# Kernel tuning notes

Hardware: AMD Instinct MI355X
Metric: run time of the kernel (lower is better)

The kernel has to match this reference:

```python
import jax, jax.numpy as jnp
import numpy as np

N, E, D, H = 50000, 800000, 64, 4  # nodes, edges, dim_h, heads
NEG_SLOPE = 0.2
BN_EPS = 1e-5


def setup_inputs() -> dict:
    key = jax.random.key(0)
    ks = jax.random.split(key, 8)
    x = jax.random.normal(ks[0], (N, D), dtype=jnp.float32)
    edge_index = jax.random.randint(ks[1], (2, E), 0, N, dtype=jnp.int32)
    s = 1.0 / np.sqrt(D)
    W_lin = jax.random.normal(ks[2], (D, D), dtype=jnp.float32) * s
    b_lin = jnp.zeros((D,), dtype=jnp.float32)
    prelu_w = jnp.full((D,), 0.25, dtype=jnp.float32)
    W_gat = jax.random.normal(ks[3], (H * D, D), dtype=jnp.float32) * s  # maps D -> H*D
    att_src = jax.random.normal(ks[4], (H, D), dtype=jnp.float32) * 0.1
    att_dst = jax.random.normal(ks[5], (H, D), dtype=jnp.float32) * 0.1
    gat_bias = jnp.zeros((D,), dtype=jnp.float32)
    bn_gamma = jnp.ones((D,), dtype=jnp.float32)
    bn_beta = jnp.zeros((D,), dtype=jnp.float32)
    return dict(x=x, edge_index=edge_index, W_lin=W_lin, b_lin=b_lin,
                prelu_w=prelu_w, W_gat=W_gat, att_src=att_src, att_dst=att_dst,
                gat_bias=gat_bias, bn_gamma=bn_gamma, bn_beta=bn_beta)


def _gat_mod_fwd(x, edge_index, W_lin, b_lin, prelu_w, W_gat, att_src, att_dst,
                 gat_bias, bn_gamma, bn_beta):
    # --- pre linear + PReLU ---
    x = x @ W_lin.T + b_lin
    x = jnp.where(x >= 0, x, prelu_w * x)  # per-channel PReLU

    # --- GATConv (concat=False -> head mean), add_self_loops=True ---
    h = (x @ W_gat.T).reshape(N, H, D)              # [N,H,D]
    a_src = jnp.einsum('nhd,hd->nh', h, att_src)    # [N,H]
    a_dst = jnp.einsum('nhd,hd->nh', h, att_dst)    # [N,H]

    loop = jnp.arange(N, dtype=edge_index.dtype)
    src = jnp.concatenate([edge_index[0], loop])    # [E+N]
    dst = jnp.concatenate([edge_index[1], loop])

    e = jax.nn.leaky_relu(a_src[src] + a_dst[dst], NEG_SLOPE)   # [E+N, H]
    # segment softmax over destination nodes (self loops guarantee non-empty)
    emax = jax.ops.segment_max(e, dst, num_segments=N)          # [N,H]
    p = jnp.exp(e - emax[dst])
    denom = jax.ops.segment_sum(p, dst, num_segments=N)         # [N,H]
    alpha = p / denom[dst]                                      # [E+N,H]

    msg = h[src] * alpha[:, :, None]                            # [E+N,H,D]
    out = jax.ops.segment_sum(msg, dst, num_segments=N)         # [N,H,D]
    out = out.mean(axis=1) + gat_bias                           # [N,D]

    # --- BatchNorm1d (training: batch stats) + ReLU ---
    mean = out.mean(axis=0)
    var = out.var(axis=0)
    out = bn_gamma * (out - mean) * jax.lax.rsqrt(var + BN_EPS) + bn_beta
    return jax.nn.relu(out)


def reference(x, edge_index, W_lin, b_lin, prelu_w, W_gat, att_src, att_dst,
              gat_bias, bn_gamma, bn_beta):
    return _gat_mod_fwd(x, edge_index, W_lin, b_lin, prelu_w, W_gat, att_src,
                        att_dst, gat_bias, bn_gamma, bn_beta)
```

## Files before the change

### kernel.cpp

```cpp
#include <hip/hip_runtime.h>
#include <hip/hip_fp16.h>

#define NEG_SLOPE 0.2f
#define BN_EPS 1e-5f

constexpr int D = 64;
constexpr int H = 4;

typedef _Float16 half2_t __attribute__((ext_vector_type(2)));
typedef _Float16 half4_t __attribute__((ext_vector_type(4)));
typedef _Float16 half8_t __attribute__((ext_vector_type(8)));
typedef float f32x4_t __attribute__((ext_vector_type(4)));
typedef int i32x4 __attribute__((ext_vector_type(4)));

union Rec {
    i32x4 i4;
    struct { int idx; int pad; half4_t w; } f;
};

#define MFMA16(a, b, c) __builtin_amdgcn_mfma_f32_16x16x32_f16(a, b, c, 0, 0, 0)

#if __has_builtin(__builtin_amdgcn_fdot2)
#define FDOT2(a, b, c) __builtin_amdgcn_fdot2((a), (b), (c), false)
#else
#define FDOT2(a, b, c) ((c) + (float)(a)[0] * (float)(b)[0] + (float)(a)[1] * (float)(b)[1])
#endif

__device__ inline half2_t h2cast(unsigned int u) { return __builtin_bit_cast(half2_t, u); }

__device__ inline float lrelu(float v) { return (v >= 0.f) ? v : NEG_SLOPE * v; }

__device__ inline void split8(const float* p, bool ok, half8_t& hi, half8_t& lo) {
    float f[8];
    if (ok) {
        float4 a = *(const float4*)p;
        float4 b = *(const float4*)(p + 4);
        f[0] = a.x; f[1] = a.y; f[2] = a.z; f[3] = a.w;
        f[4] = b.x; f[5] = b.y; f[6] = b.z; f[7] = b.w;
    } else {
        #pragma unroll
        for (int j = 0; j < 8; j++) f[j] = 0.f;
    }
    #pragma unroll
    for (int j = 0; j < 8; j++) {
        _Float16 h = (_Float16)f[j];
        hi[j] = h;
        lo[j] = (_Float16)(f[j] - (float)h);
    }
}

__global__ __launch_bounds__(256) void k_node(
    const float* __restrict__ x,
    const float* __restrict__ W_lin, const float* __restrict__ b_lin,
    const float* __restrict__ prelu_w, const float* __restrict__ W_gat,
    const float* __restrict__ att_src, const float* __restrict__ att_dst,
    _Float16* __restrict__ hh, float* __restrict__ asrc_ws,
    float* __restrict__ adst_ws, const int* __restrict__ ei,
    int* __restrict__ deg8, int* __restrict__ rank, int N, int E)
{
    __shared__ _Float16 smem[32 * 264];
    _Float16* __restrict__ h_lds = smem;
    _Float16* __restrict__ x1hi  = smem;
    _Float16* __restrict__ x1lo  = smem + 32 * 72;

    const int t = threadIdx.x;
    const int w = t >> 6;
    const int l = t & 63;
    const int li = l & 15;
    const int lq = l >> 4;
    const int base = blockIdx.x * 32;
    const int nvalid = min(32, N - base);

    const int nthreads = gridDim.x * 256;
    const int e0 = blockIdx.x * 256 + t;
    const int e1 = e0 + nthreads;
    const bool v0 = e0 < E;
    const bool v1 = e1 < E;
    const int xcd = blockIdx.x & 7;
    int r0v = 0, r1v = 0;
    {
        int d0 = 0, d1 = 0;
        if (v0) d0 = ei[E + e0];
        if (v1) d1 = ei[E + e1];
        if (v0) r0v = atomicAdd(&deg8[xcd * N + d0], 1);
        if (v1) r1v = atomicAdd(&deg8[xcd * N + d1], 1);
    }

    f32x4_t accA[2] = {};
    {
        half8_t blh[2], bll[2];
        const int n = 16 * w + li;
        #pragma unroll
        for (int ks = 0; ks < 2; ks++)
            split8(W_lin + n * 64 + 32 * ks + 8 * lq, true, blh[ks], bll[ks]);
        #pragma unroll
        for (int mt = 0; mt < 2; mt++) {
            const int row = base + 16 * mt + li;
            const bool ok = row < N;
            #pragma unroll
            for (int ks = 0; ks < 2; ks++) {
                half8_t ah, al;
                split8(x + (size_t)row * 64 + 32 * ks + 8 * lq, ok, ah, al);
                accA[mt] = MFMA16(ah, blh[ks], accA[mt]);
                accA[mt] = MFMA16(al, blh[ks], accA[mt]);
                accA[mt] = MFMA16(ah, bll[ks], accA[mt]);
            }
        }
    }

    if (v0) rank[e0] = r0v;
    if (v1) rank[e1] = r1v;

    {
        const int n = 16 * w + li;
        const float bl = b_lin[n];
        const float pw = prelu_w[n];
        #pragma unroll
        for (int mt = 0; mt < 2; mt++) {
            #pragma unroll
            for (int r = 0; r < 4; r++) {
                const int m = 16 * mt + lq * 4 + r;
                float v = accA[mt][r] + bl;
                v = (v >= 0.f) ? v : pw * v;
                _Float16 hi = (_Float16)v;
                x1hi[m * 72 + n] = hi;
                x1lo[m * 72 + n] = (_Float16)(v - (float)hi);
            }
        }
    }
    __syncthreads();

    half8_t xah[2][2], xal[2][2];
    #pragma unroll
    for (int mt = 0; mt < 2; mt++) {
        #pragma unroll
        for (int ks = 0; ks < 2; ks++) {
            const int off = (16 * mt + li) * 72 + 32 * ks + 8 * lq;
            xah[mt][ks] = *(const half8_t*)(&x1hi[off]);
            xal[mt][ks] = *(const half8_t*)(&x1lo[off]);
        }
    }
    f32x4_t accB[2][4] = {};
    #pragma unroll
    for (int nt = 0; nt < 4; nt++) {
        half8_t wh[2], wl[2];
        const int c = 64 * w + 16 * nt + li;
        #pragma unroll
        for (int ks = 0; ks < 2; ks++)
            split8(W_gat + (size_t)c * 64 + 32 * ks + 8 * lq, true, wh[ks], wl[ks]);
        #pragma unroll
        for (int mt = 0; mt < 2; mt++) {
            #pragma unroll
            for (int ks = 0; ks < 2; ks++) {
                accB[mt][nt] = MFMA16(xah[mt][ks], wh[ks], accB[mt][nt]);
                accB[mt][nt] = MFMA16(xal[mt][ks], wh[ks], accB[mt][nt]);
                accB[mt][nt] = MFMA16(xah[mt][ks], wl[ks], accB[mt][nt]);
            }
        }
    }

    {
        float asv[4], adv[4];
        #pragma unroll
        for (int nt = 0; nt < 4; nt++) {
            const int c = 64 * w + 16 * nt + li;
            asv[nt] = att_src[c];
            adv[nt] = att_dst[c];
        }
        #pragma unroll
        for (int mt = 0; mt < 2; mt++) {
            #pragma unroll
            for (int r = 0; r < 4; r++) {
                float s = 0.f, dsum = 0.f;
                #pragma unroll
                for (int nt = 0; nt < 4; nt++) {
                    s += accB[mt][nt][r] * asv[nt];
                    dsum += accB[mt][nt][r] * adv[nt];
                }
                #pragma unroll
                for (int off = 1; off < 16; off <<= 1) {
                    s += __shfl_xor(s, off, 64);
                    dsum += __shfl_xor(dsum, off, 64);
                }
                if (li == 0) {
                    const int m = 16 * mt + lq * 4 + r;
                    if (m < nvalid) {
                        asrc_ws[(size_t)(base + m) * H + w] = s;
                        adst_ws[(size_t)(base + m) * H + w] = dsum;
                    }
                }
            }
        }
    }

    __syncthreads();

    #pragma unroll
    for (int mt = 0; mt < 2; mt++) {
        #pragma unroll
        for (int nt = 0; nt < 4; nt++) {
            #pragma unroll
            for (int r = 0; r < 4; r++) {
                const int m = 16 * mt + lq * 4 + r;
                const int d = 16 * nt + li;
                h_lds[m * 264 + d * 4 + w] = (_Float16)accB[mt][nt][r];
            }
        }
    }
    __syncthreads();
    {
        const int chunks = nvalid * 32;
        const uint4* src = (const uint4*)h_lds;
        uint4* dst = (uint4*)(hh + (size_t)base * 256);
        for (int i = t; i < chunks; i += 256) {
            int row = i >> 5;
            int col = i & 31;
            dst[i] = src[row * 33 + col];
        }
    }
}

__global__ __launch_bounds__(256) void k_offsets(const int* __restrict__ deg8,
                                                 int* __restrict__ pref8,
                                                 int* __restrict__ deg,
                                                 int* __restrict__ gcount,
                                                 int* __restrict__ offs, int N) {
    __shared__ int sm[256];
    __shared__ int sbase;
    int t = threadIdx.x;
    int idx = blockIdx.x * 256 + t;
    int v = 0;
    if (idx < N) {
        #pragma unroll
        for (int p = 0; p < 8; p++) {
            int c = deg8[p * N + idx];
            pref8[p * N + idx] = v;
            v += c;
        }
        deg[idx] = v;
    }
    sm[t] = v;
    __syncthreads();
    for (int off = 1; off < 256; off <<= 1) {
        int w = (t >= off) ? sm[t - off] : 0;
        __syncthreads();
        sm[t] += w;
        __syncthreads();
    }
    if (t == 255) sbase = atomicAdd(gcount, sm[255]);
    __syncthreads();
    if (idx < N) offs[idx] = sbase + sm[t] - v;
}

__global__ __launch_bounds__(256) void k_fill(const int* __restrict__ ei,
                                              const int* __restrict__ offs,
                                              const int* __restrict__ pref8,
                                              const int* __restrict__ rank,
                                              const float* __restrict__ asrc,
                                              const float* __restrict__ adst,
                                              i32x4* __restrict__ recs,
                                              int N, int E, int NB) {
    int e = blockIdx.x * 256 + threadIdx.x;
    if (e >= E) return;
    int s = ei[e];
    int d = ei[E + e];
    int g = e >> 8;
    int p = (g < NB ? g : g - NB) & 7;
    int r0 = rank[e];
    int pos = offs[d] + pref8[p * N + d] + r0;
    float4 a = *(const float4*)(asrc + (size_t)s * H);
    float4 b = *(const float4*)(adst + (size_t)d * H);
    Rec r;
    r.f.idx = s;
    r.f.pad = 0;
    r.f.w[0] = (_Float16)__expf(lrelu(a.x + b.x));
    r.f.w[1] = (_Float16)__expf(lrelu(a.y + b.y));
    r.f.w[2] = (_Float16)__expf(lrelu(a.z + b.z));
    r.f.w[3] = (_Float16)__expf(lrelu(a.w + b.w));
    recs[pos] = r.i4;
}

__device__ inline void edge_pair(const i32x4 ra, const i32x4 rb,
                                 const uint2 ha, const uint2 hb,
                                 float& den0, float& den1, float& den2, float& den3,
                                 float& acc0, float& acc1, float& acc2, float& acc3)
{
    const half2_t one2 = h2cast(0x3C003C00u);
    unsigned int wp0 = __builtin_amdgcn_perm((unsigned int)rb.z, (unsigned int)ra.z, 0x05040100u);
    unsigned int wp1 = __builtin_amdgcn_perm((unsigned int)rb.z, (unsigned int)ra.z, 0x07060302u);
    unsigned int wp2 = __builtin_amdgcn_perm((unsigned int)rb.w, (unsigned int)ra.w, 0x05040100u);
    unsigned int wp3 = __builtin_amdgcn_perm((unsigned int)rb.w, (unsigned int)ra.w, 0x07060302u);
    unsigned int hp0 = __builtin_amdgcn_perm(hb.x, ha.x, 0x05040100u);
    unsigned int hp1 = __builtin_amdgcn_perm(hb.x, ha.x, 0x07060302u);
    unsigned int hp2 = __builtin_amdgcn_perm(hb.y, ha.y, 0x05040100u);
    unsigned int hp3 = __builtin_amdgcn_perm(hb.y, ha.y, 0x07060302u);
    den0 = FDOT2(h2cast(wp0), one2, den0);
    den1 = FDOT2(h2cast(wp1), one2, den1);
    den2 = FDOT2(h2cast(wp2), one2, den2);
    den3 = FDOT2(h2cast(wp3), one2, den3);
    acc0 = FDOT2(h2cast(wp0), h2cast(hp0), acc0);
    acc1 = FDOT2(h2cast(wp1), h2cast(hp1), acc1);
    acc2 = FDOT2(h2cast(wp2), h2cast(hp2), acc2);
    acc3 = FDOT2(h2cast(wp3), h2cast(hp3), acc3);
}

__global__ __launch_bounds__(256) void k_agg(
    const float* __restrict__ asrc, const float* __restrict__ adst,
    const int* __restrict__ offs, const int* __restrict__ deg,
    const i32x4* __restrict__ recs, const uint2* __restrict__ hh2,
    float* __restrict__ out, int N)
{
    int wid = (blockIdx.x * 256 + threadIdx.x) >> 6;
    int lane = threadIdx.x & 63;
    if (wid >= N) return;
    const int i = wid;

    float4 b = *(const float4*)(adst + (size_t)i * H);
    float4 a0 = *(const float4*)(asrc + (size_t)i * H);
    float ws0 = __expf(lrelu(a0.x + b.x));
    float ws1 = __expf(lrelu(a0.y + b.y));
    float ws2 = __expf(lrelu(a0.z + b.z));
    float ws3 = __expf(lrelu(a0.w + b.w));

    const int beg = __builtin_amdgcn_readfirstlane(offs[i]);
    const int dg  = __builtin_amdgcn_readfirstlane(deg[i]);

    float den0 = ws0, den1 = ws1, den2 = ws2, den3 = ws3;
    float acc0, acc1, acc2, acc3;
    {
        uint2 hv = hh2[(size_t)i * D + lane];
        half2_t s01 = h2cast(hv.x), s23 = h2cast(hv.y);
        acc0 = ws0 * (float)s01[0];
        acc1 = ws1 * (float)s01[1];
        acc2 = ws2 * (float)s23[0];
        acc3 = ws3 * (float)s23[1];
    }

    const int nfull = dg & ~7;
    int k = 0;
    for (; k < nfull; k += 8) {
        i32x4 rr[8];
        #pragma unroll
        for (int j = 0; j < 8; j++)
            rr[j] = __builtin_nontemporal_load(recs + beg + k + j);
        uint2 hv[8];
        #pragma unroll
        for (int j = 0; j < 8; j++)
            hv[j] = hh2[(size_t)rr[j].x * D + lane];
        #pragma unroll
        for (int j = 0; j < 8; j += 2)
            edge_pair(rr[j], rr[j + 1], hv[j], hv[j + 1],
                      den0, den1, den2, den3, acc0, acc1, acc2, acc3);
    }
    if (k < dg) {
        i32x4 rr[8];
        #pragma unroll
        for (int j = 0; j < 8; j++) {
            int kk = min(k + j, dg - 1);
            i32x4 r = __builtin_nontemporal_load(recs + beg + kk);
            if (k + j >= dg) { r.z = 0; r.w = 0; }
            rr[j] = r;
        }
        uint2 hv[8];
        #pragma unroll
        for (int j = 0; j < 8; j++)
            hv[j] = hh2[(size_t)rr[j].x * D + lane];
        #pragma unroll
        for (int j = 0; j < 8; j += 2)
            edge_pair(rr[j], rr[j + 1], hv[j], hv[j + 1],
                      den0, den1, den2, den3, acc0, acc1, acc2, acc3);
    }

    out[(size_t)i * D + lane] =
        0.25f * (acc0 / den0 + acc1 / den1 + acc2 / den2 + acc3 / den3);
}

__global__ __launch_bounds__(256) void k_bn_stats(const float* __restrict__ out,
                                                  float* __restrict__ sums,
                                                  int total) {
    const int t = threadIdx.x;
    const int stride = gridDim.x * 256;
    float s = 0.f, sq = 0.f;
    for (int idx = blockIdx.x * 256 + t; idx < total; idx += stride) {
        float v = out[idx];
        s += v;
        sq += v * v;
    }
    __shared__ float ls[256], lq[256];
    ls[t] = s;
    lq[t] = sq;
    __syncthreads();
    if (t < 64) {
        s = ls[t] + ls[t + 64] + ls[t + 128] + ls[t + 192];
        sq = lq[t] + lq[t + 64] + lq[t + 128] + lq[t + 192];
        atomicAdd(&sums[t], s);
        atomicAdd(&sums[64 + t], sq);
    }
}

__global__ __launch_bounds__(256) void k_bn_apply(float* __restrict__ out,
                                                  const float* __restrict__ sums,
                                                  const float* __restrict__ gamma,
                                                  const float* __restrict__ beta,
                                                  int total, float invN) {
    int idx = blockIdx.x * 256 + threadIdx.x;
    if (idx >= total) return;
    int c = idx & 63;
    float mean = sums[c] * invN;
    float var = sums[64 + c] * invN - mean * mean;
    float y = gamma[c] * (out[idx] - mean) * rsqrtf(var + BN_EPS) + beta[c];
    out[idx] = fmaxf(y, 0.f);
}

extern "C" void kernel_launch(void* const* d_in, const int* in_sizes, int n_in,
                              void* d_out, int out_size, void* d_ws, size_t ws_size,
                              hipStream_t stream) {
    const float* x       = (const float*)d_in[0];
    const int*   ei      = (const int*)d_in[1];
    const float* W_lin   = (const float*)d_in[2];
    const float* b_lin   = (const float*)d_in[3];
    const float* prelu_w = (const float*)d_in[4];
    const float* W_gat   = (const float*)d_in[5];
    const float* att_src = (const float*)d_in[6];
    const float* att_dst = (const float*)d_in[7];
    const float* bn_gamma = (const float*)d_in[9];
    const float* bn_beta  = (const float*)d_in[10];
    float* out = (float*)d_out;

    const int N = in_sizes[0] / D;
    const int E = in_sizes[1] / 2;

    char* wp = (char*)d_ws;
    _Float16* hh = (_Float16*)wp;      wp += (size_t)N * D * H * sizeof(_Float16);
    float* asrc  = (float*)wp;          wp += (size_t)N * H * sizeof(float);
    float* adst  = (float*)wp;          wp += (size_t)N * H * sizeof(float);
    char* zero_base = wp;
    float* sums  = (float*)wp;          wp += 2 * D * sizeof(float);
    int* deg8    = (int*)wp;            wp += (size_t)8 * N * sizeof(int);
    int* gcount  = (int*)wp;            wp += 4 * sizeof(int);
    size_t zero_bytes = (size_t)(wp - zero_base);
    int* pref8   = (int*)wp;            wp += (size_t)8 * N * sizeof(int);
    int* deg     = (int*)wp;            wp += (size_t)N * sizeof(int);
    int* offs    = (int*)wp;            wp += (size_t)N * sizeof(int);
    int* rank    = (int*)wp;            wp += (size_t)E * sizeof(int);
    i32x4* recs  = (i32x4*)wp;          wp += ((size_t)E + 4) * sizeof(i32x4);
    (void)ws_size; (void)n_in; (void)out_size;

    const int total = N * D;
    const int NB = (N + 255) / 256;
    const int NB1 = (N + 31) / 32;

    hipMemsetAsync(zero_base, 0, zero_bytes, stream);
    hipLaunchKernelGGL(k_node, dim3(NB1), dim3(256), 0, stream,
                       x, W_lin, b_lin, prelu_w, W_gat, att_src, att_dst,
                       hh, asrc, adst, ei, deg8, rank, N, E);
    hipLaunchKernelGGL(k_offsets, dim3(NB), dim3(256), 0, stream,
                       deg8, pref8, deg, gcount, offs, N);
    hipLaunchKernelGGL(k_fill, dim3((E + 255) / 256), dim3(256), 0, stream,
                       ei, offs, pref8, rank, asrc, adst, recs, N, E, NB1);
    hipLaunchKernelGGL(k_agg, dim3((N + 3) / 4), dim3(256), 0, stream,
                       asrc, adst, offs, deg, recs, (const uint2*)hh, out, N);
    hipLaunchKernelGGL(k_bn_stats, dim3(1024), dim3(256), 0, stream,
                       out, sums, total);
    hipLaunchKernelGGL(k_bn_apply, dim3((total + 255) / 256), dim3(256), 0, stream,
                       out, sums, bn_gamma, bn_beta, total, 1.f / (float)N);
}
```

Baseline: 262.7 us.

## Replace global-atomic CSR build with two-level bucketed counting sort

Drops the per-edge global atomics on per-XCD degree arrays and the rank array. The CSR is now built with a block-local LDS histogram over 32-node buckets, a three-kernel scan, a scatter into bucket order, and a per-bucket local sort into node order. It also reuses the output buffer as scratch for the intermediate records. The aim is to remove contended global atomics and scattered rank traffic. The cost is more kernel launches and an extra pass over the edge records, and the scratch reuse ties correctness to the output buffer being large enough.

```diff
diff --git a/kernel.cpp b/kernel.cpp
--- a/kernel.cpp
+++ b/kernel.cpp
@@ -6,6 +6,7 @@
 
 constexpr int D = 64;
 constexpr int H = 4;
+constexpr int MAXBUK = 1600;
 
 typedef _Float16 half2_t __attribute__((ext_vector_type(2)));
 typedef _Float16 half4_t __attribute__((ext_vector_type(4)));
@@ -55,8 +56,7 @@
     const float* __restrict__ prelu_w, const float* __restrict__ W_gat,
     const float* __restrict__ att_src, const float* __restrict__ att_dst,
     _Float16* __restrict__ hh, float* __restrict__ asrc_ws,
-    float* __restrict__ adst_ws, const int* __restrict__ ei,
-    int* __restrict__ deg8, int* __restrict__ rank, int N, int E)
+    float* __restrict__ adst_ws, int N)
 {
     __shared__ _Float16 smem[32 * 264];
     _Float16* __restrict__ h_lds = smem;
@@ -70,21 +70,6 @@
     const int lq = l >> 4;
     const int base = blockIdx.x * 32;
     const int nvalid = min(32, N - base);
-
-    const int nthreads = gridDim.x * 256;
-    const int e0 = blockIdx.x * 256 + t;
-    const int e1 = e0 + nthreads;
-    const bool v0 = e0 < E;
-    const bool v1 = e1 < E;
-    const int xcd = blockIdx.x & 7;
-    int r0v = 0, r1v = 0;
-    {
-        int d0 = 0, d1 = 0;
-        if (v0) d0 = ei[E + e0];
-        if (v1) d1 = ei[E + e1];
-        if (v0) r0v = atomicAdd(&deg8[xcd * N + d0], 1);
-        if (v1) r1v = atomicAdd(&deg8[xcd * N + d1], 1);
-    }
 
     f32x4_t accA[2] = {};
     {
@@ -107,9 +92,6 @@
             }
         }
     }
-
-    if (v0) rank[e0] = r0v;
-    if (v1) rank[e1] = r1v;
 
     {
         const int n = 16 * w + li;
@@ -220,64 +202,161 @@
     }
 }
 
-__global__ __launch_bounds__(256) void k_offsets(const int* __restrict__ deg8,
-                                                 int* __restrict__ pref8,
-                                                 int* __restrict__ deg,
-                                                 int* __restrict__ gcount,
-                                                 int* __restrict__ offs, int N) {
+__global__ __launch_bounds__(256) void k_hist(const int* __restrict__ ei,
+                                              int* __restrict__ gcnt,
+                                              int E, int chunk, int NBUK) {
+    __shared__ int cnt[MAXBUK];
+    const int p = blockIdx.x;
+    const int t = threadIdx.x;
+    for (int b = t; b < NBUK; b += 256) cnt[b] = 0;
+    __syncthreads();
+    const int e0 = p * chunk;
+    const int e1 = min(E, e0 + chunk);
+    for (int e = e0 + t; e < e1; e += 256) {
+        int d = ei[E + e];
+        atomicAdd(&cnt[d >> 5], 1);
+    }
+    __syncthreads();
+    for (int b = t; b < NBUK; b += 256) gcnt[(size_t)b * 256 + p] = cnt[b];
+}
+
+__global__ __launch_bounds__(256) void k_scan1(const int* __restrict__ gcnt,
+                                               int* __restrict__ tot, int NBUK) {
+    const int b = blockIdx.x * 4 + (threadIdx.x >> 6);
+    const int l = threadIdx.x & 63;
+    if (b >= NBUK) return;
+    int4 v = ((const int4*)(gcnt + (size_t)b * 256))[l];
+    int s = v.x + v.y + v.z + v.w;
+    #pragma unroll
+    for (int off = 1; off < 64; off <<= 1) s += __shfl_xor(s, off, 64);
+    if (l == 0) tot[b] = s;
+}
+
+__global__ __launch_bounds__(256) void k_scan2(const int* __restrict__ tot,
+                                               int* __restrict__ base, int NBUK) {
     __shared__ int sm[256];
-    __shared__ int sbase;
-    int t = threadIdx.x;
-    int idx = blockIdx.x * 256 + t;
-    int v = 0;
-    if (idx < N) {
-        #pragma unroll
-        for (int p = 0; p < 8; p++) {
-            int c = deg8[p * N + idx];
-            pref8[p * N + idx] = v;
-            v += c;
-        }
-        deg[idx] = v;
-    }
-    sm[t] = v;
-    __syncthreads();
-    for (int off = 1; off < 256; off <<= 1) {
-        int w = (t >= off) ? sm[t - off] : 0;
+    __shared__ int carry_s;
+    const int t = threadIdx.x;
+    if (t == 0) carry_s = 0;
+    __syncthreads();
+    for (int c0 = 0; c0 < NBUK; c0 += 256) {
+        const int i = c0 + t;
+        const int v = (i < NBUK) ? tot[i] : 0;
+        sm[t] = v;
         __syncthreads();
-        sm[t] += w;
+        for (int off = 1; off < 256; off <<= 1) {
+            int u = (t >= off) ? sm[t - off] : 0;
+            __syncthreads();
+            sm[t] += u;
+            __syncthreads();
+        }
+        const int inc = sm[t];
+        const int cc = carry_s;
         __syncthreads();
-    }
-    if (t == 255) sbase = atomicAdd(gcount, sm[255]);
-    __syncthreads();
-    if (idx < N) offs[idx] = sbase + sm[t] - v;
-}
-
-__global__ __launch_bounds__(256) void k_fill(const int* __restrict__ ei,
-                                              const int* __restrict__ offs,
-                                              const int* __restrict__ pref8,
-                                              const int* __restrict__ rank,
-                                              const float* __restrict__ asrc,
-                                              const float* __restrict__ adst,
-                                              i32x4* __restrict__ recs,
-                                              int N, int E, int NB) {
-    int e = blockIdx.x * 256 + threadIdx.x;
-    if (e >= E) return;
-    int s = ei[e];
-    int d = ei[E + e];
-    int g = e >> 8;
-    int p = (g < NB ? g : g - NB) & 7;
-    int r0 = rank[e];
-    int pos = offs[d] + pref8[p * N + d] + r0;
-    float4 a = *(const float4*)(asrc + (size_t)s * H);
-    float4 b = *(const float4*)(adst + (size_t)d * H);
-    Rec r;
-    r.f.idx = s;
-    r.f.pad = 0;
-    r.f.w[0] = (_Float16)__expf(lrelu(a.x + b.x));
-    r.f.w[1] = (_Float16)__expf(lrelu(a.y + b.y));
-    r.f.w[2] = (_Float16)__expf(lrelu(a.z + b.z));
-    r.f.w[3] = (_Float16)__expf(lrelu(a.w + b.w));
-    recs[pos] = r.i4;
+        if (t == 255) carry_s = cc + sm[255];
+        if (i < NBUK) base[i] = cc + inc - v;
+        __syncthreads();
+    }
+    if (t == 0) base[NBUK] = carry_s;
+}
+
+__global__ __launch_bounds__(256) void k_scan3(int* __restrict__ gcnt,
+                                               const int* __restrict__ base,
+                                               int NBUK) {
+    const int b = blockIdx.x * 4 + (threadIdx.x >> 6);
+    const int l = threadIdx.x & 63;
+    if (b >= NBUK) return;
+    int4 v = ((int4*)(gcnt + (size_t)b * 256))[l];
+    int s = v.x + v.y + v.z + v.w;
+    int inc = s;
+    #pragma unroll
+    for (int off = 1; off < 64; off <<= 1) {
+        int u = __shfl_up(inc, off, 64);
+        if (l >= off) inc += u;
+    }
+    int ex = base[b] + inc - s;
+    int4 o;
+    o.x = ex;
+    o.y = ex + v.x;
+    o.z = o.y + v.y;
+    o.w = o.z + v.z;
+    ((int4*)(gcnt + (size_t)b * 256))[l] = o;
+}
+
+__global__ __launch_bounds__(256) void k_fillB(const int* __restrict__ ei,
+                                               const int* __restrict__ gcnt,
+                                               const float* __restrict__ asrc,
+                                               const float* __restrict__ adst,
+                                               i32x4* __restrict__ recsA,
+                                               int E, int chunk, int NBUK) {
+    __shared__ int cur[MAXBUK];
+    const int p = blockIdx.x;
+    const int t = threadIdx.x;
+    for (int b = t; b < NBUK; b += 256) cur[b] = 0;
+    __syncthreads();
+    const int e0 = p * chunk;
+    const int e1 = min(E, e0 + chunk);
+    for (int e = e0 + t; e < e1; e += 256) {
+        int s = ei[e];
+        int d = ei[E + e];
+        int b = d >> 5;
+        int lr = atomicAdd(&cur[b], 1);
+        int pos = gcnt[(size_t)b * 256 + p] + lr;
+        float4 a = *(const float4*)(asrc + (size_t)s * H);
+        float4 bb = *(const float4*)(adst + (size_t)d * H);
+        Rec r;
+        r.f.idx = s;
+        r.f.pad = d;
+        r.f.w[0] = (_Float16)__expf(lrelu(a.x + bb.x));
+        r.f.w[1] = (_Float16)__expf(lrelu(a.y + bb.y));
+        r.f.w[2] = (_Float16)__expf(lrelu(a.z + bb.z));
+        r.f.w[3] = (_Float16)__expf(lrelu(a.w + bb.w));
+        recsA[pos] = r.i4;
+    }
+}
+
+__global__ __launch_bounds__(256) void k_fillC(const i32x4* __restrict__ recsA,
+                                               const int* __restrict__ base,
+                                               i32x4* __restrict__ recsB,
+                                               int* __restrict__ offs,
+                                               int* __restrict__ deg,
+                                               int N, int NBUK) {
+    const int b = blockIdx.x;
+    const int t = threadIdx.x;
+    __shared__ int c32[32], s32[32], cu32[32];
+    const int lo = base[b];
+    const int hi = base[b + 1];
+    if (t < 32) { c32[t] = 0; cu32[t] = 0; }
+    __syncthreads();
+    for (int i = lo + t; i < hi; i += 256) {
+        Rec r;
+        r.i4 = recsA[i];
+        atomicAdd(&c32[r.f.pad & 31], 1);
+    }
+    __syncthreads();
+    if (t < 32) {
+        int v = c32[t];
+        int inc = v;
+        #pragma unroll
+        for (int off = 1; off < 32; off <<= 1) {
+            int u = __shfl_up(inc, off, 64);
+            if (t >= off) inc += u;
+        }
+        s32[t] = lo + inc - v;
+        int node = b * 32 + t;
+        if (node < N) {
+            offs[node] = lo + inc - v;
+            deg[node] = v;
+        }
+    }
+    __syncthreads();
+    for (int i = lo + t; i < hi; i += 256) {
+        Rec r;
+        r.i4 = recsA[i];
+        int n = r.f.pad & 31;
+        int slot = atomicAdd(&cu32[n], 1);
+        recsB[s32[n] + slot] = r.i4;
+    }
 }
 
 __device__ inline void edge_pair(const i32x4 ra, const i32x4 rb,
@@ -429,37 +508,50 @@
 
     const int N = in_sizes[0] / D;
     const int E = in_sizes[1] / 2;
+    const int NBUK = (N + 31) / 32;
+    const int chunk = (E + 255) / 256;
 
     char* wp = (char*)d_ws;
     _Float16* hh = (_Float16*)wp;      wp += (size_t)N * D * H * sizeof(_Float16);
     float* asrc  = (float*)wp;          wp += (size_t)N * H * sizeof(float);
     float* adst  = (float*)wp;          wp += (size_t)N * H * sizeof(float);
-    char* zero_base = wp;
     float* sums  = (float*)wp;          wp += 2 * D * sizeof(float);
-    int* deg8    = (int*)wp;            wp += (size_t)8 * N * sizeof(int);
-    int* gcount  = (int*)wp;            wp += 4 * sizeof(int);
-    size_t zero_bytes = (size_t)(wp - zero_base);
-    int* pref8   = (int*)wp;            wp += (size_t)8 * N * sizeof(int);
+    int* gcnt    = (int*)wp;            wp += (size_t)NBUK * 256 * sizeof(int);
+    int* tot     = (int*)wp;            wp += (size_t)((NBUK + 3) & ~3) * sizeof(int);
+    int* basep   = (int*)wp;            wp += (size_t)((NBUK + 4) & ~3) * sizeof(int);
+    int* offs    = (int*)wp;            wp += (size_t)N * sizeof(int);
     int* deg     = (int*)wp;            wp += (size_t)N * sizeof(int);
-    int* offs    = (int*)wp;            wp += (size_t)N * sizeof(int);
-    int* rank    = (int*)wp;            wp += (size_t)E * sizeof(int);
-    i32x4* recs  = (i32x4*)wp;          wp += ((size_t)E + 4) * sizeof(i32x4);
-    (void)ws_size; (void)n_in; (void)out_size;
+    i32x4* recsB = (i32x4*)wp;          wp += (size_t)E * sizeof(i32x4);
+    i32x4* recsA;
+    if ((size_t)E * sizeof(i32x4) <= (size_t)out_size) {
+        recsA = (i32x4*)d_out;
+    } else {
+        recsA = (i32x4*)wp;             wp += (size_t)E * sizeof(i32x4);
+    }
+    (void)ws_size; (void)n_in;
 
     const int total = N * D;
-    const int NB = (N + 255) / 256;
     const int NB1 = (N + 31) / 32;
-
-    hipMemsetAsync(zero_base, 0, zero_bytes, stream);
+    const int NBW = (NBUK + 3) / 4;
+
+    hipMemsetAsync(sums, 0, 2 * D * sizeof(float), stream);
     hipLaunchKernelGGL(k_node, dim3(NB1), dim3(256), 0, stream,
                        x, W_lin, b_lin, prelu_w, W_gat, att_src, att_dst,
-                       hh, asrc, adst, ei, deg8, rank, N, E);
-    hipLaunchKernelGGL(k_offsets, dim3(NB), dim3(256), 0, stream,
-                       deg8, pref8, deg, gcount, offs, N);
-    hipLaunchKernelGGL(k_fill, dim3((E + 255) / 256), dim3(256), 0, stream,
-                       ei, offs, pref8, rank, asrc, adst, recs, N, E, NB1);
+                       hh, asrc, adst, N);
+    hipLaunchKernelGGL(k_hist, dim3(256), dim3(256), 0, stream,
+                       ei, gcnt, E, chunk, NBUK);
+    hipLaunchKernelGGL(k_scan1, dim3(NBW), dim3(256), 0, stream,
+                       gcnt, tot, NBUK);
+    hipLaunchKernelGGL(k_scan2, dim3(1), dim3(256), 0, stream,
+                       tot, basep, NBUK);
+    hipLaunchKernelGGL(k_scan3, dim3(NBW), dim3(256), 0, stream,
+                       gcnt, basep, NBUK);
+    hipLaunchKernelGGL(k_fillB, dim3(256), dim3(256), 0, stream,
+                       ei, gcnt, asrc, adst, recsA, E, chunk, NBUK);
+    hipLaunchKernelGGL(k_fillC, dim3(NBUK), dim3(256), 0, stream,
+                       recsA, basep, recsB, offs, deg, N, NBUK);
     hipLaunchKernelGGL(k_agg, dim3((N + 3) / 4), dim3(256), 0, stream,
-                       asrc, adst, offs, deg, recs, (const uint2*)hh, out, N);
+                       asrc, adst, offs, deg, recsB, (const uint2*)hh, out, N);
     hipLaunchKernelGGL(k_bn_stats, dim3(1024), dim3(256), 0, stream,
                        out, sums, total);
     hipLaunchKernelGGL(k_bn_apply, dim3((total + 255) / 256), dim3(256), 0, stream,
```

Measured after the change: 257.7 us. Within noise of the previous version (-1.9%).

## Build CSR with LDS chunked histograms instead of global per-XCD atomics

Applied to the files above, without the earlier changes.

Edge bucketing by destination moves out of k_node, which no longer does global atomicAdd counting or writes a per-edge rank array. A new k_hist kernel counts destinations in shared memory per edge chunk, in two passes over node halves, using packed 16-bit counters. A per-chunk exclusive prefix in k_off then yields node offsets and degrees, and k_fill recomputes local ranks with LDS atomics to scatter records. This is meant to cut global atomic contention and the rank/pref8 traffic. In exchange it reads the edge list twice more, does a serial 128-step prefix per word, and borrows the output buffer as scratch for the chunk-count table.

```diff
diff --git a/kernel.cpp b/kernel.cpp
--- a/kernel.cpp
+++ b/kernel.cpp
@@ -6,6 +6,9 @@
 
 constexpr int D = 64;
 constexpr int H = 4;
+
+constexpr int PSORT = 128;
+constexpr int MAXW2 = 12544;
 
 typedef _Float16 half2_t __attribute__((ext_vector_type(2)));
 typedef _Float16 half4_t __attribute__((ext_vector_type(4)));
@@ -55,8 +58,7 @@
     const float* __restrict__ prelu_w, const float* __restrict__ W_gat,
     const float* __restrict__ att_src, const float* __restrict__ att_dst,
     _Float16* __restrict__ hh, float* __restrict__ asrc_ws,
-    float* __restrict__ adst_ws, const int* __restrict__ ei,
-    int* __restrict__ deg8, int* __restrict__ rank, int N, int E)
+    float* __restrict__ adst_ws, int N)
 {
     __shared__ _Float16 smem[32 * 264];
     _Float16* __restrict__ h_lds = smem;
@@ -70,21 +72,6 @@
     const int lq = l >> 4;
     const int base = blockIdx.x * 32;
     const int nvalid = min(32, N - base);
-
-    const int nthreads = gridDim.x * 256;
-    const int e0 = blockIdx.x * 256 + t;
-    const int e1 = e0 + nthreads;
-    const bool v0 = e0 < E;
-    const bool v1 = e1 < E;
-    const int xcd = blockIdx.x & 7;
-    int r0v = 0, r1v = 0;
-    {
-        int d0 = 0, d1 = 0;
-        if (v0) d0 = ei[E + e0];
-        if (v1) d1 = ei[E + e1];
-        if (v0) r0v = atomicAdd(&deg8[xcd * N + d0], 1);
-        if (v1) r1v = atomicAdd(&deg8[xcd * N + d1], 1);
-    }
 
     f32x4_t accA[2] = {};
     {
@@ -107,9 +94,6 @@
             }
         }
     }
-
-    if (v0) rank[e0] = r0v;
-    if (v1) rank[e1] = r1v;
 
     {
         const int n = 16 * w + li;
@@ -220,64 +204,105 @@
     }
 }
 
-__global__ __launch_bounds__(256) void k_offsets(const int* __restrict__ deg8,
-                                                 int* __restrict__ pref8,
-                                                 int* __restrict__ deg,
-                                                 int* __restrict__ gcount,
-                                                 int* __restrict__ offs, int N) {
+__global__ __launch_bounds__(1024) void k_hist(const int* __restrict__ ei,
+                                               unsigned int* __restrict__ gcnt,
+                                               int E, int chunk, int N2, int WTOT) {
+    __shared__ unsigned int cnt[MAXW2];
+    const int p = blockIdx.x & (PSORT - 1);
+    const int pass = blockIdx.x >> 7;
+    const int t = threadIdx.x;
+    const int W2 = N2 >> 1;
+    for (int i = t; i < W2; i += 1024) cnt[i] = 0;
+    __syncthreads();
+    const int e0 = p * chunk;
+    const int e1 = min(E, e0 + chunk);
+    const int nlo = pass * N2;
+    for (int e = e0 + t; e < e1; e += 1024) {
+        int dl = ei[E + e] - nlo;
+        if ((unsigned)dl < (unsigned)N2)
+            atomicAdd(&cnt[dl >> 1], 1u << ((dl & 1) * 16));
+    }
+    __syncthreads();
+    unsigned int* dst = gcnt + (size_t)p * WTOT + (size_t)pass * W2;
+    for (int i = t; i < W2; i += 1024) dst[i] = cnt[i];
+}
+
+__global__ __launch_bounds__(256) void k_off(unsigned int* __restrict__ gcnt,
+                                             int* __restrict__ gcount,
+                                             int* __restrict__ offs,
+                                             int* __restrict__ deg,
+                                             int N, int WTOT) {
     __shared__ int sm[256];
     __shared__ int sbase;
-    int t = threadIdx.x;
-    int idx = blockIdx.x * 256 + t;
-    int v = 0;
-    if (idx < N) {
-        #pragma unroll
-        for (int p = 0; p < 8; p++) {
-            int c = deg8[p * N + idx];
-            pref8[p * N + idx] = v;
-            v += c;
-        }
-        deg[idx] = v;
-    }
+    const int t = threadIdx.x;
+    const int i = blockIdx.x * 256 + t;
+    int d0 = 0, d1 = 0;
+    if (i < WTOT) {
+        unsigned int run = 0;
+        for (int p = 0; p < PSORT; p++) {
+            unsigned int* q = gcnt + (size_t)p * WTOT + i;
+            unsigned int c = *q;
+            *q = run;
+            run += c;
+        }
+        d0 = (int)(run & 0xffffu);
+        d1 = (int)(run >> 16);
+    }
+    int v = d0 + d1;
     sm[t] = v;
     __syncthreads();
     for (int off = 1; off < 256; off <<= 1) {
-        int w = (t >= off) ? sm[t - off] : 0;
+        int u = (t >= off) ? sm[t - off] : 0;
         __syncthreads();
-        sm[t] += w;
+        sm[t] += u;
         __syncthreads();
     }
     if (t == 255) sbase = atomicAdd(gcount, sm[255]);
     __syncthreads();
-    if (idx < N) offs[idx] = sbase + sm[t] - v;
-}
-
-__global__ __launch_bounds__(256) void k_fill(const int* __restrict__ ei,
-                                              const int* __restrict__ offs,
-                                              const int* __restrict__ pref8,
-                                              const int* __restrict__ rank,
-                                              const float* __restrict__ asrc,
-                                              const float* __restrict__ adst,
-                                              i32x4* __restrict__ recs,
-                                              int N, int E, int NB) {
-    int e = blockIdx.x * 256 + threadIdx.x;
-    if (e >= E) return;
-    int s = ei[e];
-    int d = ei[E + e];
-    int g = e >> 8;
-    int p = (g < NB ? g : g - NB) & 7;
-    int r0 = rank[e];
-    int pos = offs[d] + pref8[p * N + d] + r0;
-    float4 a = *(const float4*)(asrc + (size_t)s * H);
-    float4 b = *(const float4*)(adst + (size_t)d * H);
-    Rec r;
-    r.f.idx = s;
-    r.f.pad = 0;
-    r.f.w[0] = (_Float16)__expf(lrelu(a.x + b.x));
-    r.f.w[1] = (_Float16)__expf(lrelu(a.y + b.y));
-    r.f.w[2] = (_Float16)__expf(lrelu(a.z + b.z));
-    r.f.w[3] = (_Float16)__expf(lrelu(a.w + b.w));
-    recs[pos] = r.i4;
+    const int base = sbase + sm[t] - v;
+    const int n0 = 2 * i;
+    if (n0 < N)     { offs[n0] = base;          deg[n0] = d0; }
+    if (n0 + 1 < N) { offs[n0 + 1] = base + d0; deg[n0 + 1] = d1; }
+}
+
+__global__ __launch_bounds__(1024) void k_fill(const int* __restrict__ ei,
+                                               const unsigned int* __restrict__ gcnt,
+                                               const int* __restrict__ offs,
+                                               const float* __restrict__ asrc,
+                                               const float* __restrict__ adst,
+                                               i32x4* __restrict__ recs,
+                                               int E, int chunk, int N2, int WTOT) {
+    __shared__ unsigned int cur[MAXW2];
+    const int p = blockIdx.x & (PSORT - 1);
+    const int pass = blockIdx.x >> 7;
+    const int t = threadIdx.x;
+    const int W2 = N2 >> 1;
+    for (int i = t; i < W2; i += 1024) cur[i] = 0;
+    __syncthreads();
+    const int e0 = p * chunk;
+    const int e1 = min(E, e0 + chunk);
+    const int nlo = pass * N2;
+    for (int e = e0 + t; e < e1; e += 1024) {
+        int d = ei[E + e];
+        int dl = d - nlo;
+        if ((unsigned)dl >= (unsigned)N2) continue;
+        int s = ei[e];
+        const unsigned int sh = (unsigned)(dl & 1) * 16;
+        unsigned int old = atomicAdd(&cur[dl >> 1], 1u << sh);
+        int lr = (int)((old >> sh) & 0xffffu);
+        int pr = (int)((gcnt[(size_t)p * WTOT + (d >> 1)] >> sh) & 0xffffu);
+        int pos = offs[d] + pr + lr;
+        float4 a = *(const float4*)(asrc + (size_t)s * H);
+        float4 b = *(const float4*)(adst + (size_t)d * H);
+        Rec r;
+        r.f.idx = s;
+        r.f.pad = 0;
+        r.f.w[0] = (_Float16)__expf(lrelu(a.x + b.x));
+        r.f.w[1] = (_Float16)__expf(lrelu(a.y + b.y));
+        r.f.w[2] = (_Float16)__expf(lrelu(a.z + b.z));
+        r.f.w[3] = (_Float16)__expf(lrelu(a.w + b.w));
+        recs[pos] = r.i4;
+    }
 }
 
 __device__ inline void edge_pair(const i32x4 ra, const i32x4 rb,
@@ -430,34 +455,46 @@
     const int N = in_sizes[0] / D;
     const int E = in_sizes[1] / 2;
 
+    int N2 = (N + 1) / 2;
+    N2 = (N2 + 1) & ~1;
+    const int WTOT = N2;
+    const int chunk = (E + PSORT - 1) / PSORT;
+
     char* wp = (char*)d_ws;
     _Float16* hh = (_Float16*)wp;      wp += (size_t)N * D * H * sizeof(_Float16);
     float* asrc  = (float*)wp;          wp += (size_t)N * H * sizeof(float);
     float* adst  = (float*)wp;          wp += (size_t)N * H * sizeof(float);
     char* zero_base = wp;
     float* sums  = (float*)wp;          wp += 2 * D * sizeof(float);
-    int* deg8    = (int*)wp;            wp += (size_t)8 * N * sizeof(int);
     int* gcount  = (int*)wp;            wp += 4 * sizeof(int);
     size_t zero_bytes = (size_t)(wp - zero_base);
-    int* pref8   = (int*)wp;            wp += (size_t)8 * N * sizeof(int);
-    int* deg     = (int*)wp;            wp += (size_t)N * sizeof(int);
-    int* offs    = (int*)wp;            wp += (size_t)N * sizeof(int);
-    int* rank    = (int*)wp;            wp += (size_t)E * sizeof(int);
-    i32x4* recs  = (i32x4*)wp;          wp += ((size_t)E + 4) * sizeof(i32x4);
-    (void)ws_size; (void)n_in; (void)out_size;
+    int* offs    = (int*)wp;            wp += (size_t)((N + 3) & ~3) * sizeof(int);
+    int* deg     = (int*)wp;            wp += (size_t)((N + 3) & ~3) * sizeof(int);
+    i32x4* recs  = (i32x4*)wp;          wp += (size_t)E * sizeof(i32x4);
+    unsigned int* gcnt;
+    if ((size_t)PSORT * WTOT * sizeof(unsigned int) <= (size_t)out_size) {
+        gcnt = (unsigned int*)d_out;
+    } else {
+        gcnt = (unsigned int*)wp;
+        wp += (size_t)PSORT * WTOT * sizeof(unsigned int);
+    }
+    (void)ws_size; (void)n_in;
 
     const int total = N * D;
-    const int NB = (N + 255) / 256;
     const int NB1 = (N + 31) / 32;
+    const int NBS = 2 * PSORT;
+    const int NBO = (WTOT + 255) / 256;
 
     hipMemsetAsync(zero_base, 0, zero_bytes, stream);
     hipLaunchKernelGGL(k_node, dim3(NB1), dim3(256), 0, stream,
                        x, W_lin, b_lin, prelu_w, W_gat, att_src, att_dst,
-                       hh, asrc, adst, ei, deg8, rank, N, E);
-    hipLaunchKernelGGL(k_offsets, dim3(NB), dim3(256), 0, stream,
-                       deg8, pref8, deg, gcount, offs, N);
-    hipLaunchKernelGGL(k_fill, dim3((E + 255) / 256), dim3(256), 0, stream,
-                       ei, offs, pref8, rank, asrc, adst, recs, N, E, NB1);
+                       hh, asrc, adst, N);
+    hipLaunchKernelGGL(k_hist, dim3(NBS), dim3(1024), 0, stream,
+                       ei, gcnt, E, chunk, N2, WTOT);
+    hipLaunchKernelGGL(k_off, dim3(NBO), dim3(256), 0, stream,
+                       gcnt, gcount, offs, deg, N, WTOT);
+    hipLaunchKernelGGL(k_fill, dim3(NBS), dim3(1024), 0, stream,
+                       ei, gcnt, offs, asrc, adst, recs, E, chunk, N2, WTOT);
     hipLaunchKernelGGL(k_agg, dim3((N + 3) / 4), dim3(256), 0, stream,
                        asrc, adst, offs, deg, recs, (const uint2*)hh, out, N);
     hipLaunchKernelGGL(k_bn_stats, dim3(1024), dim3(256), 0, stream,
```

New measurement: 261.6 us. Within noise of the previous version (-0.4%).
